# Optimization experiments

Measured on AMD Instinct MI355X. Metric: run time of the kernel, lower is better.

## Reference

```python
import math
import jax, jax.numpy as jnp
import numpy as np

B, S, D, H = 4, 1024, 512, 8
DK = D // H


def lin(x, W, b):
    # torch nn.Linear: y = x @ W.T + b, W: [out, in]
    return jnp.einsum('...i,oi->...o', x, W) + b


def layer_norm(x, scale, bias, eps=1e-5):
    m = jnp.mean(x, axis=-1, keepdims=True)
    v = jnp.var(x, axis=-1, keepdims=True)
    return (x - m) / jnp.sqrt(v + eps) * scale + bias


def mha(q_in, k_in, v_in, Wq, bq, Wk, bk, Wv, bv, Wo, bo, gammas, mask, zero_pad):
    b, s, _ = q_in.shape
    q = lin(q_in, Wq, bq).reshape(b, s, H, DK).transpose(0, 2, 1, 3)  # bhsd
    k = lin(k_in, Wk, bk).reshape(b, s, H, DK).transpose(0, 2, 1, 3)
    v = lin(v_in, Wv, bv).reshape(b, s, H, DK).transpose(0, 2, 1, 3)
    scores = jnp.einsum('bhid,bhjd->bhij', q, k) / math.sqrt(DK)
    # no-grad distance-decay branch
    s_ = jnp.where(mask, scores, jnp.float32(-1e32))
    s_ = jax.nn.softmax(s_, axis=-1) * mask
    distcum = jnp.cumsum(s_, axis=-1)
    disttotal = jnp.sum(s_, axis=-1, keepdims=True)
    idx = jnp.arange(s)
    pos = jnp.abs(idx[None, :] - idx[:, None]).astype(jnp.float32)[None, None]  # |i-j|
    dist = jax.lax.stop_gradient(jnp.sqrt(jnp.clip((disttotal - distcum) * pos, 0.0, None)))
    gamma = -jax.nn.softplus(gammas)[None]  # [1,h,1,1]
    total_effect = jnp.clip(jnp.exp(dist * gamma), 1e-5, 1e5)
    scores = scores * total_effect
    # NOTE: original code calls scores.masked_fill(...) without assignment (no-op);
    # faithfully NOT re-masking before this softmax.
    att = jax.nn.softmax(scores, axis=-1)
    if zero_pad:
        att = att.at[:, :, 0, :].set(0.0)
    out = jnp.einsum('bhij,bhjd->bhid', att, v).transpose(0, 2, 1, 3).reshape(b, s, D)
    return lin(out, Wo, bo)


def setup_inputs() -> dict:
    key = jax.random.key(0)
    ks = jax.random.split(key, 32)
    ki = iter(range(32))

    def w(shape, scale=0.02):
        return jax.random.normal(ks[next(ki)], shape, jnp.float32) * scale

    inp = {
        'q_emb': jax.random.normal(ks[next(ki)], (B, S, D), jnp.float32),
        'qa_emb': jax.random.normal(ks[next(ki)], (B, S, D), jnp.float32),
    }
    for blk in (1, 2, 3):
        inp[f'Wq{blk}'] = w((D, D)); inp[f'bq{blk}'] = jnp.zeros((D,), jnp.float32)
        if blk == 3:
            inp['Wk3'] = w((D, D)); inp['bk3'] = jnp.zeros((D,), jnp.float32)
        inp[f'Wv{blk}'] = w((D, D)); inp[f'bv{blk}'] = jnp.zeros((D,), jnp.float32)
        inp[f'Wo{blk}'] = w((D, D)); inp[f'bo{blk}'] = jnp.zeros((D,), jnp.float32)
        inp[f'g{blk}'] = w((H, 1, 1), 0.5)
        inp[f'ls{blk}'] = jnp.ones((D,), jnp.float32)
        inp[f'lb{blk}'] = jnp.zeros((D,), jnp.float32)
    inp['know'] = jax.random.uniform(ks[next(ki)], (1, 1, D), jnp.float32, -1.0, 1.0)
    inp['Wlk'] = w((D, DK)); inp['b_lk'] = jnp.zeros((D,), jnp.float32)
    inp['Wlv'] = w((D, DK)); inp['b_lv'] = jnp.zeros((D,), jnp.float32)
    return inp


def reference(q_emb, qa_emb,
              Wq1, bq1, Wv1, bv1, Wo1, bo1, g1, ls1, lb1,
              Wq2, bq2, Wv2, bv2, Wo2, bo2, g2, ls2, lb2,
              Wq3, bq3, Wk3, bk3, Wv3, bv3, Wo3, bo3, g3, ls3, lb3,
              know, Wlk, b_lk, Wlv, b_lv):
    b, s, d = q_emb.shape
    ones = jnp.ones((s, s), dtype=bool)
    mask_peek = jnp.tril(ones, k=0)[None, None]   # peek_cur=True
    mask_nopeek = jnp.tril(ones, k=-1)[None, None]  # peek_cur=False

    # block1 / block2 share k and q projections (kq_same=True)
    hq = layer_norm(q_emb + mha(q_emb, q_emb, q_emb, Wq1, bq1, Wq1, bq1,
                                Wv1, bv1, Wo1, bo1, g1, mask_peek, False), ls1, lb1)
    ha = layer_norm(qa_emb + mha(qa_emb, qa_emb, qa_emb, Wq2, bq2, Wq2, bq2,
                                 Wv2, bv2, Wo2, bo2, g2, mask_peek, False), ls2, lb2)
    query = jnp.broadcast_to(know, (b, s, d))
    h = layer_norm(query + mha(query, hq, ha, Wq3, bq3, Wk3, bk3,
                               Wv3, bv3, Wo3, bo3, g3, mask_nopeek, True), ls3, lb3)

    # small multi-head combine
    key_t = jax.nn.sigmoid(lin(query.reshape(b, s, H, DK), Wlk, b_lk))  # [b,s,h,d]
    val_t = jax.nn.sigmoid(lin(h.reshape(b, s, H, DK), Wlv, b_lv))     # [b,s,h,d]
    beta = jnp.einsum('bshd,bsd->bsh', key_t, q_emb)
    alpha = jax.nn.softmax(beta, axis=-1)
    out = jnp.einsum('bsh,bshd->bsd', alpha, val_t)
    return out
```

## Files before the change

### kernel.cpp

```cpp
#include <hip/hip_runtime.h>
#include <math.h>

#define BB 4
#define S 1024
#define D 512
#define H 8
#define DKH 64

#define ATT_LD 1032
#define LOG2E 1.4426950408889634f

typedef __attribute__((ext_vector_type(8))) short bf16x8;
typedef __attribute__((ext_vector_type(4))) float f32x4;

__device__ __forceinline__ unsigned short f2bf(float f){
  unsigned int u = __float_as_uint(f);
  u += 0x7FFFu + ((u >> 16) & 1u);
  return (unsigned short)(u >> 16);
}
__device__ __forceinline__ float bf2f(unsigned int v){
  return __uint_as_float(v << 16);
}
__device__ __forceinline__ f32x4 MFMA(bf16x8 a, bf16x8 b, f32x4 c){
  return __builtin_amdgcn_mfma_f32_16x16x32_bf16(a, b, c, 0, 0, 0);
}
__device__ __forceinline__ void gl_lds16(const void* g, void* l){
  __builtin_amdgcn_global_load_lds(
      (const __attribute__((address_space(1))) void*)g,
      (__attribute__((address_space(3))) void*)l, 16, 0, 0);
}

__device__ __forceinline__ float blk_sum(float* r, int t, float v){
  r[t] = v; __syncthreads();
  for (int s = 128; s > 0; s >>= 1){
    if (t < s) r[t] += r[t + s];
    __syncthreads();
  }
  float res = r[0]; __syncthreads();
  return res;
}

struct GemmJobs {
  const unsigned short* A[4];
  const unsigned short* W[4];
  const float* bias[4];
  void* C[4];
};
template<int OUTBF>
__global__ __launch_bounds__(256) void mfma_gemm_b(GemmJobs jb)
{
  __shared__ __align__(16) short As[128][32];
  __shared__ __align__(16) short Ws[128][32];
  const int t = threadIdx.x;
  const int z = blockIdx.z;
  const int n0 = blockIdx.x * 128, m0 = blockIdx.y * 128;
  const unsigned short* A = jb.A[z];
  const unsigned short* W = jb.W[z];
  const float* bias = jb.bias[z];
  const int w = t >> 6, lane = t & 63;
  const int wm = (w >> 1) << 6, wn = (w & 1) << 6;
  const int lm = lane & 15, q = lane >> 4;
  const int r = t >> 2, cc = (t & 3) << 3;
  char* ldsA = ((char*)&As[0][0]) + w * 1024;
  char* ldsW = ((char*)&Ws[0][0]) + w * 1024;
  f32x4 acc[4][4];
  #pragma unroll
  for (int a_ = 0; a_ < 4; a_++)
    #pragma unroll
    for (int b_ = 0; b_ < 4; b_++)
      acc[a_][b_] = (f32x4){0.f, 0.f, 0.f, 0.f};
  for (int k0 = 0; k0 < D; k0 += 32){
    gl_lds16(&A[(size_t)(m0 + r)      * D + k0 + cc], ldsA);
    gl_lds16(&A[(size_t)(m0 + r + 64) * D + k0 + cc], ldsA + 4096);
    gl_lds16(&W[(size_t)(n0 + r)      * D + k0 + cc], ldsW);
    gl_lds16(&W[(size_t)(n0 + r + 64) * D + k0 + cc], ldsW + 4096);
    __syncthreads();
    bf16x8 af[4], bf[4];
    #pragma unroll
    for (int mt = 0; mt < 4; mt++) af[mt] = *(const bf16x8*)&As[wm + mt*16 + lm][q*8];
    #pragma unroll
    for (int nt = 0; nt < 4; nt++) bf[nt] = *(const bf16x8*)&Ws[wn + nt*16 + lm][q*8];
    #pragma unroll
    for (int mt = 0; mt < 4; mt++)
      #pragma unroll
      for (int nt = 0; nt < 4; nt++)
        acc[mt][nt] = MFMA(af[mt], bf[nt], acc[mt][nt]);
    __syncthreads();
  }
  #pragma unroll
  for (int nt = 0; nt < 4; nt++){
    const int n = n0 + wn + nt*16 + lm;
    const float bs = bias[n];
    #pragma unroll
    for (int mt = 0; mt < 4; mt++){
      const int mb = m0 + wm + mt*16 + (q << 2);
      f32x4 c = acc[mt][nt];
      #pragma unroll
      for (int rr = 0; rr < 4; rr++){
        float vv = c[rr] + bs;
        if (OUTBF)
          ((unsigned short*)jb.C[z])[(size_t)(mb + rr) * D + n] = f2bf(vv);
        else
          ((float*)jb.C[z])[(size_t)(mb + rr) * D + n] = vv;
      }
    }
  }
}

#define KS_LD 66
struct VTArgs { const unsigned short* v[2]; unsigned short* vt[2]; };
__global__ __launch_bounds__(256) void vt_kernel(VTArgs a)
{
  __shared__ unsigned short tile[64 * KS_LD];
  const int z = blockIdx.z, bh = blockIdx.y, b = bh >> 3, h = bh & 7;
  const int j0 = blockIdx.x * 64;
  const int t = threadIdx.x;
  const unsigned short* vp = a.v[z];
  unsigned short* vtp = a.vt[z] + (size_t)bh * 64 * S;
  #pragma unroll
  for (int p = 0; p < 2; p++){
    int lin = t + p * 256, row = lin >> 3, c8 = (lin & 7) << 3;
    *(uint4*)&tile[row * KS_LD + c8] =
      *(const uint4*)&vp[((size_t)b * S + j0 + row) * D + h * DKH + c8];
  }
  __syncthreads();
  #pragma unroll
  for (int p = 0; p < 2; p++){
    int lin = t + p * 256, d = lin >> 3, c8 = (lin & 7) << 3;
    unsigned short tmp[8];
    #pragma unroll
    for (int jx = 0; jx < 8; jx++) tmp[jx] = tile[(c8 + jx) * KS_LD + d];
    *(uint4*)&vtp[(size_t)d * S + j0 + c8] = *(const uint4*)tmp;
  }
}

struct FAArgs {
  const unsigned short* qk[2];
  const unsigned short* vt[2];
  unsigned short* ctx[2];
  const float* g[2];
  const float* c3;
  int diag, zero_pad;
};
template<int C3>
__global__ __launch_bounds__(256) void fused_attn(FAArgs a)
{
  __shared__ __align__(16) unsigned short att[16 * ATT_LD];
  const int t = threadIdx.x;
  const int z = blockIdx.z;
  const int bh = blockIdx.y, b = bh >> 3, h = bh & 7;
  const int i0 = blockIdx.x * 16;
  const int w = t >> 6, lane = t & 63, lm = lane & 15, q = lane >> 4;
  const unsigned short* qkp = a.qk[z];
  const unsigned short* vtp = a.vt[z] + (size_t)bh * 64 * S;
  unsigned short* ctxp = a.ctx[z];
  float gm2;
  { float gv = a.g[z][h];
    gm2 = -((gv > 20.f) ? gv : log1pf(expf(gv))) * LOG2E; }

  if (!C3){
    bf16x8 af0 = *(const bf16x8*)&qkp[((size_t)b * S + i0 + lm) * D + h * DKH + q*8];
    bf16x8 af1 = *(const bf16x8*)&qkp[((size_t)b * S + i0 + lm) * D + h * DKH + 32 + q*8];
    for (int jc = 0; jc < S; jc += 64){
      const int jrow = jc + w*16 + lm;
      const size_t kb = ((size_t)b * S + jrow) * D + h * DKH;
      bf16x8 bv0 = *(const bf16x8*)&qkp[kb + q*8];
      bf16x8 bv1 = *(const bf16x8*)&qkp[kb + 32 + q*8];
      f32x4 acc = (f32x4){0.f, 0.f, 0.f, 0.f};
      acc = MFMA(af0, bv0, acc);
      acc = MFMA(af1, bv1, acc);
      #pragma unroll
      for (int rr = 0; rr < 4; rr++)
        att[(q*4 + rr) * ATT_LD + jc + w*16 + lm] = f2bf(acc[rr] * 0.125f);
    }
  }
  __syncthreads();

  const int jA0 = lane * 8, jB0 = 512 + lane * 8;
  for (int rloc = 0; rloc < 4; rloc++){
    const int i = i0 + w*4 + rloc;
    unsigned short* rowp = &att[(w*4 + rloc) * ATT_LD];
    if (C3 && a.zero_pad && i == 0){
      uint4 zz = make_uint4(0u,0u,0u,0u);
      *(uint4*)&rowp[jA0] = zz;
      *(uint4*)&rowp[jB0] = zz;
      continue;
    }
    float c[16];
    if (C3){
      const float* c3p = a.c3 + ((size_t)b * H + h) * S;
      #pragma unroll
      for (int sg = 0; sg < 2; sg++)
        #pragma unroll
        for (int p4 = 0; p4 < 2; p4++){
          float4 x = *(const float4*)&c3p[sg*512 + lane*8 + p4*4];
          c[sg*8+p4*4+0] = x.x * LOG2E; c[sg*8+p4*4+1] = x.y * LOG2E;
          c[sg*8+p4*4+2] = x.z * LOG2E; c[sg*8+p4*4+3] = x.w * LOG2E;
        }
    } else {
      #pragma unroll
      for (int sg = 0; sg < 2; sg++){
        uint4 u = *(const uint4*)&rowp[sg*512 + lane*8];
        unsigned int uu[4] = {u.x, u.y, u.z, u.w};
        #pragma unroll
        for (int mel = 0; mel < 4; mel++){
          c[sg*8 + mel*2]     = bf2f(uu[mel] & 0xffffu) * LOG2E;
          c[sg*8 + mel*2 + 1] = bf2f(uu[mel] >> 16) * LOG2E;
        }
      }
    }
    const int jmax = i + a.diag;
    float pl[16];
    float runA = 0.f, runB = 0.f;
    #pragma unroll
    for (int k = 0; k < 8; k++){
      float e = (jA0 + k <= jmax) ? exp2f(c[k]) : 0.f;
      runA += e; pl[k] = runA;
    }
    #pragma unroll
    for (int k = 0; k < 8; k++){
      float e = (jB0 + k <= jmax) ? exp2f(c[8+k]) : 0.f;
      runB += e; pl[8+k] = runB;
    }
    float sA = runA, sB = runB;
    #pragma unroll
    for (int off = 1; off < 64; off <<= 1){
      float uA = __shfl_up(sA, off, 64);
      float uB = __shfl_up(sB, off, 64);
      if (lane >= off){ sA += uA; sB += uB; }
    }
    const float TA = __shfl(sA, 63, 64);
    const float T  = TA + __shfl(sB, 63, 64);
    const float inv1 = 1.f / T;
    const float cbaseA = (T - (sA - runA)) * inv1;
    const float cbaseB = (T - (TA + sB - runB)) * inv1;
    const float fiA = (float)(i - jA0);
    const float fiB = (float)(i - jB0);
    float ls2 = 0.f;
    #pragma unroll
    for (int k = 0; k < 8; k++){
      float remn = fmaf(-pl[k], inv1, cbaseA);
      float pos  = fabsf(fiA - (float)k);
      float dist = sqrtf(fmaxf(remn * pos, 0.f));
      float eff  = fmaxf(exp2f(gm2 * dist), 1e-5f);
      float pp   = exp2f(c[k] * eff);
      ls2 += pp; pl[k] = pp;
    }
    #pragma unroll
    for (int k = 0; k < 8; k++){
      float remn = fmaf(-pl[8+k], inv1, cbaseB);
      float pos  = fabsf(fiB - (float)k);
      float dist = sqrtf(fmaxf(remn * pos, 0.f));
      float eff  = fmaxf(exp2f(gm2 * dist), 1e-5f);
      float pp   = exp2f(c[8+k] * eff);
      ls2 += pp; pl[8+k] = pp;
    }
    #pragma unroll
    for (int off = 1; off < 64; off <<= 1) ls2 += __shfl_xor(ls2, off, 64);
    const float inv2 = 1.f / ls2;
    #pragma unroll
    for (int sg = 0; sg < 2; sg++){
      unsigned int ou[4];
      #pragma unroll
      for (int mel = 0; mel < 4; mel++){
        unsigned int lo = f2bf(pl[sg*8 + 2*mel]     * inv2);
        unsigned int hi = f2bf(pl[sg*8 + 2*mel + 1] * inv2);
        ou[mel] = lo | (hi << 16);
      }
      *(uint4*)&rowp[sg*512 + lane*8] = make_uint4(ou[0], ou[1], ou[2], ou[3]);
    }
  }
  __syncthreads();

  f32x4 acc = (f32x4){0.f,0.f,0.f,0.f};
  for (int kc = 0; kc < S; kc += 64){
    #pragma unroll
    for (int kft = 0; kft < 2; kft++){
      bf16x8 afv = *(const bf16x8*)&att[lm * ATT_LD + kc + kft*32 + q*8];
      bf16x8 bv  = *(const bf16x8*)&vtp[(size_t)(w*16 + lm) * S + kc + kft*32 + q*8];
      acc = MFMA(afv, bv, acc);
    }
  }
  #pragma unroll
  for (int rr = 0; rr < 4; rr++){
    const int row = i0 + q*4 + rr;
    ctxp[((size_t)b * S + row) * D + h * DKH + w*16 + lm] = f2bf(acc[rr]);
  }
}

__global__ __launch_bounds__(256) void ln_residual(
    const float* __restrict__ resid, const float* __restrict__ y,
    const float* __restrict__ ls, const float* __restrict__ lb,
    unsigned short* __restrict__ out, int bcast)
{
  const int r = blockIdx.x, t = threadIdx.x;
  __shared__ float red[256];
  const size_t base = (size_t)r * D;
  float r0 = bcast ? resid[t]       : resid[base + t];
  float r1 = bcast ? resid[t + 256] : resid[base + t + 256];
  float x0 = r0 + y[base + t];
  float x1 = r1 + y[base + t + 256];
  float mean = blk_sum(red, t, x0 + x1) * (1.0f / 512.0f);
  float d0 = x0 - mean, d1 = x1 - mean;
  float var = blk_sum(red, t, d0*d0 + d1*d1) * (1.0f / 512.0f);
  float inv = rsqrtf(var + 1e-5f);
  out[base + t]       = f2bf(d0 * inv * ls[t]       + lb[t]);
  out[base + t + 256] = f2bf(d1 * inv * ls[t + 256] + lb[t + 256]);
}

struct CvtJobs {
  const float* s[12];
  unsigned short* d[12];
  int n[12];
};
__global__ __launch_bounds__(256) void cvt_all(CvtJobs jb){
  const int z = blockIdx.y;
  const int n = jb.n[z];
  const float* s = jb.s[z];
  unsigned short* d = jb.d[z];
  for (int idx = blockIdx.x * 256 + threadIdx.x; idx < n; idx += gridDim.x * 256)
    d[idx] = f2bf(s[idx]);
}

__global__ __launch_bounds__(256) void qvec3_kernel(
    const float* __restrict__ know, const float* __restrict__ Wq3,
    const float* __restrict__ bq3, float* __restrict__ q3)
{
  const int wv = (blockIdx.x * 256 + threadIdx.x) >> 6;
  const int lane = threadIdx.x & 63;
  const float* wr = Wq3 + (size_t)wv * 512 + lane * 8;
  const float* kr = know + lane * 8;
  float4 w0 = *(const float4*)&wr[0], w1 = *(const float4*)&wr[4];
  float4 k0 = *(const float4*)&kr[0], k1 = *(const float4*)&kr[4];
  float p = w0.x*k0.x + w0.y*k0.y + w0.z*k0.z + w0.w*k0.w
          + w1.x*k1.x + w1.y*k1.y + w1.z*k1.z + w1.w*k1.w;
  #pragma unroll
  for (int off = 1; off < 64; off <<= 1) p += __shfl_xor(p, off, 64);
  if (lane == 0) q3[wv] = p + bq3[wv];
}

__global__ __launch_bounds__(256) void keyt_kernel(
    const float* __restrict__ know, const float* __restrict__ Wlk,
    const float* __restrict__ blk_, float* __restrict__ keyt)
{
  int idx = blockIdx.x * 256 + threadIdx.x;
  int h = idx >> 9, n = idx & 511;
  float acc = 0.f;
  for (int i = 0; i < 64; i++) acc += know[h * 64 + i] * Wlk[(size_t)n * 64 + i];
  keyt[idx] = 1.f / (1.f + __expf(-(acc + blk_[n])));
}

__global__ __launch_bounds__(256) void scores3_kernel(
    const float* __restrict__ q3, const unsigned short* __restrict__ k3,
    float* __restrict__ c3)
{
  int idx = blockIdx.x * 256 + threadIdx.x;
  int j  = idx & (S - 1);
  int bh = idx >> 10;
  int h  = bh & 7, b = bh >> 3;
  const unsigned short* kp = k3 + ((size_t)b * S + j) * D + h * DKH;
  const float* qp = q3 + h * DKH;
  float acc = 0.f;
  #pragma unroll
  for (int d8 = 0; d8 < 64; d8 += 8){
    uint4 u = *(const uint4*)&kp[d8];
    unsigned int uu[4] = {u.x, u.y, u.z, u.w};
    #pragma unroll
    for (int mel = 0; mel < 4; mel++){
      acc += qp[d8 + 2*mel]     * bf2f(uu[mel] & 0xffffu);
      acc += qp[d8 + 2*mel + 1] * bf2f(uu[mel] >> 16);
    }
  }
  c3[idx] = acc * 0.125f;
}

__global__ __launch_bounds__(256) void alphas_kernel(
    const float* __restrict__ keyt, const float* __restrict__ q_emb,
    float* __restrict__ alpha)
{
  const int row = blockIdx.x * 4 + (threadIdx.x >> 6);
  const int l = threadIdx.x & 63;
  const int h = l >> 3, sub = l & 7;
  const float* qr = q_emb + (size_t)row * D;
  const float* kt = keyt + h * D;
  float p = 0.f;
  for (int d = sub; d < D; d += 8) p += kt[d] * qr[d];
  p += __shfl_xor(p, 1, 64);
  p += __shfl_xor(p, 2, 64);
  p += __shfl_xor(p, 4, 64);
  float m = p;
  m = fmaxf(m, __shfl_xor(m, 8, 64));
  m = fmaxf(m, __shfl_xor(m, 16, 64));
  m = fmaxf(m, __shfl_xor(m, 32, 64));
  float e = __expf(p - m);
  float ssum = e;
  ssum += __shfl_xor(ssum, 8, 64);
  ssum += __shfl_xor(ssum, 16, 64);
  ssum += __shfl_xor(ssum, 32, 64);
  if (sub == 0) alpha[(size_t)row * H + h] = e / ssum;
}

__global__ __launch_bounds__(256) void val_fused(
    const unsigned short* __restrict__ Ah,
    const unsigned short* __restrict__ Wv,
    const float* __restrict__ blv,
    const float* __restrict__ alpha,
    float* __restrict__ out)
{
  __shared__ __align__(16) short As[128][32];
  __shared__ __align__(16) short Ws[128][32];
  __shared__ float als[128];
  const int t = threadIdx.x;
  const int n0 = blockIdx.x * 128, m0 = blockIdx.y * 128;
  if (t < 128) als[t] = alpha[m0 + t];
  const int w = t >> 6, lane = t & 63;
  const int wm = (w >> 1) << 6, wn = (w & 1) << 6;
  const int lm = lane & 15, q = lane >> 4;
  const int r = t >> 2, cc = (t & 3) << 3;
  f32x4 acc[4][4];
  #pragma unroll
  for (int a_ = 0; a_ < 4; a_++)
    #pragma unroll
    for (int b_ = 0; b_ < 4; b_++)
      acc[a_][b_] = (f32x4){0.f, 0.f, 0.f, 0.f};
  for (int k0 = 0; k0 < 64; k0 += 32){
    *(uint4*)&As[r][cc]      = *(const uint4*)&Ah[(size_t)(m0 + r) * 64 + k0 + cc];
    *(uint4*)&As[r + 64][cc] = *(const uint4*)&Ah[(size_t)(m0 + r + 64) * 64 + k0 + cc];
    *(uint4*)&Ws[r][cc]      = *(const uint4*)&Wv[(size_t)(n0 + r) * 64 + k0 + cc];
    *(uint4*)&Ws[r + 64][cc] = *(const uint4*)&Wv[(size_t)(n0 + r + 64) * 64 + k0 + cc];
    __syncthreads();
    bf16x8 af[4], bf[4];
    #pragma unroll
    for (int mt = 0; mt < 4; mt++) af[mt] = *(const bf16x8*)&As[wm + mt*16 + lm][q*8];
    #pragma unroll
    for (int nt = 0; nt < 4; nt++) bf[nt] = *(const bf16x8*)&Ws[wn + nt*16 + lm][q*8];
    #pragma unroll
    for (int mt = 0; mt < 4; mt++)
      #pragma unroll
      for (int nt = 0; nt < 4; nt++)
        acc[mt][nt] = MFMA(af[mt], bf[nt], acc[mt][nt]);
    __syncthreads();
  }
  #pragma unroll
  for (int nt = 0; nt < 4; nt++){
    const int n = n0 + wn + nt*16 + lm;
    const float bs = blv[n];
    #pragma unroll
    for (int mt = 0; mt < 4; mt++){
      const int mb = m0 + wm + mt*16;
      f32x4 c = acc[mt][nt];
      float part = 0.f;
      #pragma unroll
      for (int rr = 0; rr < 4; rr++){
        const int ml = (mb - m0) + (q << 2) + rr;
        float sg = 1.f / (1.f + __expf(-(c[rr] + bs)));
        part += als[ml] * sg;
      }
      part += __shfl_xor(part, 16, 64);
      if ((q & 1) == 0){
        const int srow = (mb >> 3) + (q >> 1);
        out[(size_t)srow * D + n] = part;
      }
    }
  }
}

extern "C" void kernel_launch(void* const* d_in, const int* in_sizes, int n_in,
                              void* d_out, int out_size, void* d_ws, size_t ws_size,
                              hipStream_t stream) {
  const float* q_emb  = (const float*)d_in[0];
  const float* qa_emb = (const float*)d_in[1];
  const float* Wq1 = (const float*)d_in[2],  *bq1 = (const float*)d_in[3];
  const float* Wv1 = (const float*)d_in[4],  *bv1 = (const float*)d_in[5];
  const float* Wo1 = (const float*)d_in[6],  *bo1 = (const float*)d_in[7];
  const float* g1  = (const float*)d_in[8],  *ls1 = (const float*)d_in[9],  *lb1 = (const float*)d_in[10];
  const float* Wq2 = (const float*)d_in[11], *bq2 = (const float*)d_in[12];
  const float* Wv2 = (const float*)d_in[13], *bv2 = (const float*)d_in[14];
  const float* Wo2 = (const float*)d_in[15], *bo2 = (const float*)d_in[16];
  const float* g2  = (const float*)d_in[17], *ls2 = (const float*)d_in[18], *lb2 = (const float*)d_in[19];
  const float* Wq3 = (const float*)d_in[20], *bq3 = (const float*)d_in[21];
  const float* Wk3 = (const float*)d_in[22], *bk3 = (const float*)d_in[23];
  const float* Wv3 = (const float*)d_in[24], *bv3 = (const float*)d_in[25];
  const float* Wo3 = (const float*)d_in[26], *bo3 = (const float*)d_in[27];
  const float* g3  = (const float*)d_in[28], *ls3 = (const float*)d_in[29], *lb3 = (const float*)d_in[30];
  const float* know = (const float*)d_in[31];
  const float* Wlk  = (const float*)d_in[32], *b_lk = (const float*)d_in[33];
  const float* Wlv  = (const float*)d_in[34], *b_lv = (const float*)d_in[35];
  float* outp = (float*)d_out;

  const size_t NSD = (size_t)BB * S * D;
  unsigned short* p = (unsigned short*)d_ws;
  unsigned short* qk1b = p; p += NSD;
  unsigned short* v1b  = p; p += NSD;
  unsigned short* qk2b = p; p += NSD;
  unsigned short* v2b  = p; p += NSD;
  unsigned short* k3b  = p; p += NSD;
  unsigned short* v3b  = p; p += NSD;
  unsigned short* ctx1b= p; p += NSD;
  unsigned short* ctx2b= p; p += NSD;
  unsigned short* ctx3b= p; p += NSD;
  unsigned short* xqb  = p; p += NSD;
  unsigned short* xab  = p; p += NSD;
  unsigned short* hqb  = p; p += NSD;
  unsigned short* hab  = p; p += NSD;
  unsigned short* hfb  = p; p += NSD;
  unsigned short* vt1  = p; p += NSD;
  unsigned short* vt2  = p; p += NSD;
  unsigned short* vt3  = p; p += NSD;
  unsigned short* wb   = p; p += (size_t)9 * D * D;
  unsigned short* wlvb = p; p += (size_t)D * DKH;
  float* yv0   = (float*)p;
  float* yv1   = yv0 + NSD;
  float* q3    = yv1 + NSD;
  float* keyt  = q3 + 512;
  float* c3    = keyt + 4096;
  float* alpha = c3 + (size_t)BB * H * S;

  unsigned short* Wq1b = wb + 0*(size_t)D*D;
  unsigned short* Wv1b = wb + 1*(size_t)D*D;
  unsigned short* Wo1b = wb + 2*(size_t)D*D;
  unsigned short* Wq2b = wb + 3*(size_t)D*D;
  unsigned short* Wv2b = wb + 4*(size_t)D*D;
  unsigned short* Wo2b = wb + 5*(size_t)D*D;
  unsigned short* Wk3b = wb + 6*(size_t)D*D;
  unsigned short* Wv3b = wb + 7*(size_t)D*D;
  unsigned short* Wo3b = wb + 8*(size_t)D*D;

  CvtJobs jb;
  jb.s[0] = q_emb;  jb.d[0] = xqb;  jb.n[0] = (int)NSD;
  jb.s[1] = qa_emb; jb.d[1] = xab;  jb.n[1] = (int)NSD;
  jb.s[2] = Wq1; jb.d[2] = Wq1b; jb.n[2] = D*D;
  jb.s[3] = Wv1; jb.d[3] = Wv1b; jb.n[3] = D*D;
  jb.s[4] = Wo1; jb.d[4] = Wo1b; jb.n[4] = D*D;
  jb.s[5] = Wq2; jb.d[5] = Wq2b; jb.n[5] = D*D;
  jb.s[6] = Wv2; jb.d[6] = Wv2b; jb.n[6] = D*D;
  jb.s[7] = Wo2; jb.d[7] = Wo2b; jb.n[7] = D*D;
  jb.s[8] = Wk3; jb.d[8] = Wk3b; jb.n[8] = D*D;
  jb.s[9] = Wv3; jb.d[9] = Wv3b; jb.n[9] = D*D;
  jb.s[10] = Wo3; jb.d[10] = Wo3b; jb.n[10] = D*D;
  jb.s[11] = Wlv; jb.d[11] = wlvb; jb.n[11] = D*DKH;
  cvt_all<<<dim3(256, 12), 256, 0, stream>>>(jb);

  {
    GemmJobs g;
    g.A[0]=xqb; g.W[0]=Wq1b; g.bias[0]=bq1; g.C[0]=qk1b;
    g.A[1]=xqb; g.W[1]=Wv1b; g.bias[1]=bv1; g.C[1]=v1b;
    g.A[2]=xab; g.W[2]=Wq2b; g.bias[2]=bq2; g.C[2]=qk2b;
    g.A[3]=xab; g.W[3]=Wv2b; g.bias[3]=bv2; g.C[3]=v2b;
    mfma_gemm_b<1><<<dim3(4, 32, 4), 256, 0, stream>>>(g);
  }
  { VTArgs a; a.v[0]=v1b; a.v[1]=v2b; a.vt[0]=vt1; a.vt[1]=vt2;
    vt_kernel<<<dim3(16, 32, 2), 256, 0, stream>>>(a); }
  { FAArgs a;
    a.qk[0]=qk1b; a.qk[1]=qk2b; a.vt[0]=vt1; a.vt[1]=vt2;
    a.ctx[0]=ctx1b; a.ctx[1]=ctx2b; a.g[0]=g1; a.g[1]=g2;
    a.c3=nullptr; a.diag=0; a.zero_pad=0;
    fused_attn<0><<<dim3(64, 32, 2), 256, 0, stream>>>(a); }
  {
    GemmJobs g;
    g.A[0]=ctx1b; g.W[0]=Wo1b; g.bias[0]=bo1; g.C[0]=yv0;
    g.A[1]=ctx2b; g.W[1]=Wo2b; g.bias[1]=bo2; g.C[1]=yv1;
    g.A[2]=ctx1b; g.W[2]=Wo1b; g.bias[2]=bo1; g.C[2]=yv0;
    g.A[3]=ctx1b; g.W[3]=Wo1b; g.bias[3]=bo1; g.C[3]=yv0;
    mfma_gemm_b<0><<<dim3(4, 32, 2), 256, 0, stream>>>(g);
  }
  ln_residual<<<BB*S, 256, 0, stream>>>(q_emb,  yv0, ls1, lb1, hqb, 0);
  ln_residual<<<BB*S, 256, 0, stream>>>(qa_emb, yv1, ls2, lb2, hab, 0);

  qvec3_kernel<<<128, 256, 0, stream>>>(know, Wq3, bq3, q3);
  {
    GemmJobs g;
    g.A[0]=hqb; g.W[0]=Wk3b; g.bias[0]=bk3; g.C[0]=k3b;
    g.A[1]=hab; g.W[1]=Wv3b; g.bias[1]=bv3; g.C[1]=v3b;
    g.A[2]=hqb; g.W[2]=Wk3b; g.bias[2]=bk3; g.C[2]=k3b;
    g.A[3]=hqb; g.W[3]=Wk3b; g.bias[3]=bk3; g.C[3]=k3b;
    mfma_gemm_b<1><<<dim3(4, 32, 2), 256, 0, stream>>>(g);
  }
  { VTArgs a; a.v[0]=v3b; a.v[1]=v3b; a.vt[0]=vt3; a.vt[1]=vt3;
    vt_kernel<<<dim3(16, 32, 1), 256, 0, stream>>>(a); }
  scores3_kernel<<<128, 256, 0, stream>>>(q3, k3b, c3);
  { FAArgs a;
    a.qk[0]=k3b; a.qk[1]=k3b; a.vt[0]=vt3; a.vt[1]=vt3;
    a.ctx[0]=ctx3b; a.ctx[1]=ctx3b; a.g[0]=g3; a.g[1]=g3;
    a.c3=c3; a.diag=-1; a.zero_pad=1;
    fused_attn<1><<<dim3(64, 32, 1), 256, 0, stream>>>(a); }
  {
    GemmJobs g;
    g.A[0]=ctx3b; g.W[0]=Wo3b; g.bias[0]=bo3; g.C[0]=yv0;
    g.A[1]=ctx3b; g.W[1]=Wo3b; g.bias[1]=bo3; g.C[1]=yv0;
    g.A[2]=ctx3b; g.W[2]=Wo3b; g.bias[2]=bo3; g.C[2]=yv0;
    g.A[3]=ctx3b; g.W[3]=Wo3b; g.bias[3]=bo3; g.C[3]=yv0;
    mfma_gemm_b<0><<<dim3(4, 32, 1), 256, 0, stream>>>(g);
  }
  ln_residual<<<BB*S, 256, 0, stream>>>(know, yv0, ls3, lb3, hfb, 1);

  keyt_kernel<<<16, 256, 0, stream>>>(know, Wlk, b_lk, keyt);
  alphas_kernel<<<1024, 256, 0, stream>>>(keyt, q_emb, alpha);
  val_fused<<<dim3(4, 256), 256, 0, stream>>>(hfb, wlvb, b_lv, alpha, outp);
}
```

Measured before the change: 478.8 us.

## Streamline decay softmax: skip masked half, defer normalization, batch small kernels

Inside fused attention, the upper-half scan and decay evaluation are skipped when the causal row limit lies below column 512. The row normalization is deferred to the attention-times-V epilogue through a shared per-row reciprocal, and faster bf16 rounding, hardware exp2/sqrt/rcp intrinsics and hoisted C3 exponentials are used. Separately, the two layer-norm launches are batched into one grid and the q3/keyt kernels are merged into a single launch to cut launch overhead. The skipped half writes unnormalized exp values instead of decayed ones, which could alter results, and the approximate intrinsics and round-half-up conversion change numerics slightly.

```diff
diff --git a/kernel.cpp b/kernel.cpp
--- a/kernel.cpp
+++ b/kernel.cpp
@@ -13,10 +13,38 @@
 typedef __attribute__((ext_vector_type(8))) short bf16x8;
 typedef __attribute__((ext_vector_type(4))) float f32x4;
 
+#if __has_builtin(__builtin_amdgcn_exp2f)
+#define EXP2(x) __builtin_amdgcn_exp2f(x)
+#else
+#define EXP2(x) exp2f(x)
+#endif
+#if __has_builtin(__builtin_amdgcn_sqrtf)
+#define SQRTF(x) __builtin_amdgcn_sqrtf(x)
+#else
+#define SQRTF(x) sqrtf(x)
+#endif
+#if __has_builtin(__builtin_amdgcn_rcpf)
+#define RCPF(x) __builtin_amdgcn_rcpf(x)
+#else
+#define RCPF(x) (1.0f / (x))
+#endif
+
 __device__ __forceinline__ unsigned short f2bf(float f){
   unsigned int u = __float_as_uint(f);
   u += 0x7FFFu + ((u >> 16) & 1u);
   return (unsigned short)(u >> 16);
+}
+__device__ __forceinline__ unsigned short f2bf_rhu(float f){
+  return (unsigned short)((__float_as_uint(f) + 0x8000u) >> 16);
+}
+__device__ __forceinline__ unsigned int pk_rhu(float lo, float hi){
+  unsigned int a = __float_as_uint(lo) + 0x8000u;
+  unsigned int b = __float_as_uint(hi) + 0x8000u;
+#if __has_builtin(__builtin_amdgcn_perm)
+  return __builtin_amdgcn_perm(b, a, 0x07060302u);
+#else
+  return (a >> 16) | (b & 0xffff0000u);
+#endif
 }
 __device__ __forceinline__ float bf2f(unsigned int v){
   return __uint_as_float(v << 16);
@@ -146,6 +174,7 @@
 __global__ __launch_bounds__(256) void fused_attn(FAArgs a)
 {
   __shared__ __align__(16) unsigned short att[16 * ATT_LD];
+  __shared__ float ls2s[16];
   const int t = threadIdx.x;
   const int z = blockIdx.z;
   const int bh = blockIdx.y, b = bh >> 3, h = bh & 7;
@@ -171,33 +200,119 @@
       acc = MFMA(af1, bv1, acc);
       #pragma unroll
       for (int rr = 0; rr < 4; rr++)
-        att[(q*4 + rr) * ATT_LD + jc + w*16 + lm] = f2bf(acc[rr] * 0.125f);
+        att[(q*4 + rr) * ATT_LD + jc + w*16 + lm] = f2bf_rhu(acc[rr] * 0.125f);
     }
   }
   __syncthreads();
 
   const int jA0 = lane * 8, jB0 = 512 + lane * 8;
+
+  float cH[16], erH[16];
+  if (C3){
+    const float* c3p = a.c3 + ((size_t)b * H + h) * S;
+    #pragma unroll
+    for (int sg = 0; sg < 2; sg++)
+      #pragma unroll
+      for (int p4 = 0; p4 < 2; p4++){
+        float4 x = *(const float4*)&c3p[sg*512 + lane*8 + p4*4];
+        cH[sg*8+p4*4+0] = x.x * LOG2E; cH[sg*8+p4*4+1] = x.y * LOG2E;
+        cH[sg*8+p4*4+2] = x.z * LOG2E; cH[sg*8+p4*4+3] = x.w * LOG2E;
+      }
+    #pragma unroll
+    for (int k = 0; k < 16; k++) erH[k] = EXP2(cH[k]);
+  }
+
+  auto decay_row = [&](const float (&c)[16], const float (&er)[16],
+                       const int i, unsigned short* rowp, const int rl){
+    const int jmax = i + a.diag;
+    const bool skipB = (jmax < 512);
+    float pl[16];
+    float runA = 0.f;
+    #pragma unroll
+    for (int k = 0; k < 8; k++){
+      float e = (jA0 + k <= jmax) ? er[k] : 0.f;
+      runA += e; pl[k] = runA;
+    }
+    float sA = runA;
+    #pragma unroll
+    for (int off = 1; off < 64; off <<= 1){
+      float u = __shfl_up(sA, off, 64);
+      if (lane >= off) sA += u;
+    }
+    const float TA = __shfl(sA, 63, 64);
+    float T = TA, sB = 0.f, runB = 0.f;
+    if (!skipB){
+      #pragma unroll
+      for (int k = 0; k < 8; k++){
+        float e = (jB0 + k <= jmax) ? er[8+k] : 0.f;
+        runB += e; pl[8+k] = runB;
+      }
+      sB = runB;
+      #pragma unroll
+      for (int off = 1; off < 64; off <<= 1){
+        float u = __shfl_up(sB, off, 64);
+        if (lane >= off) sB += u;
+      }
+      T = TA + __shfl(sB, 63, 64);
+    }
+    const float inv1 = RCPF(T);
+    const float cbaseA = (T - (sA - runA)) * inv1;
+    const float fiA = (float)(i - jA0);
+    float ls2 = 0.f;
+    #pragma unroll
+    for (int k = 0; k < 8; k++){
+      float remn = fmaf(-pl[k], inv1, cbaseA);
+      float pos  = fabsf(fiA - (float)k);
+      float dist = SQRTF(fmaxf(remn * pos, 0.f));
+      float eff  = fmaxf(EXP2(gm2 * dist), 1e-5f);
+      float pp   = EXP2(c[k] * eff);
+      ls2 += pp; pl[k] = pp;
+    }
+    if (!skipB){
+      const float cbaseB = (T - (TA + sB - runB)) * inv1;
+      const float fiB = (float)(i - jB0);
+      #pragma unroll
+      for (int k = 0; k < 8; k++){
+        float remn = fmaf(-pl[8+k], inv1, cbaseB);
+        float pos  = fabsf(fiB - (float)k);
+        float dist = SQRTF(fmaxf(remn * pos, 0.f));
+        float eff  = fmaxf(EXP2(gm2 * dist), 1e-5f);
+        float pp   = EXP2(c[8+k] * eff);
+        ls2 += pp; pl[8+k] = pp;
+      }
+    } else {
+      #pragma unroll
+      for (int k = 0; k < 8; k++){ pl[8+k] = er[8+k]; ls2 += er[8+k]; }
+    }
+    #pragma unroll
+    for (int off = 1; off < 64; off <<= 1) ls2 += __shfl_xor(ls2, off, 64);
+    if (lane == 0) ls2s[rl] = RCPF(ls2);
+    #pragma unroll
+    for (int sg = 0; sg < 2; sg++){
+      uint4 o;
+      o.x = pk_rhu(pl[sg*8+0], pl[sg*8+1]);
+      o.y = pk_rhu(pl[sg*8+2], pl[sg*8+3]);
+      o.z = pk_rhu(pl[sg*8+4], pl[sg*8+5]);
+      o.w = pk_rhu(pl[sg*8+6], pl[sg*8+7]);
+      *(uint4*)&rowp[sg*512 + lane*8] = o;
+    }
+  };
+
   for (int rloc = 0; rloc < 4; rloc++){
-    const int i = i0 + w*4 + rloc;
-    unsigned short* rowp = &att[(w*4 + rloc) * ATT_LD];
+    const int rl = w*4 + rloc;
+    const int i = i0 + rl;
+    unsigned short* rowp = &att[rl * ATT_LD];
     if (C3 && a.zero_pad && i == 0){
       uint4 zz = make_uint4(0u,0u,0u,0u);
       *(uint4*)&rowp[jA0] = zz;
       *(uint4*)&rowp[jB0] = zz;
+      if (lane == 0) ls2s[0] = 1.f;
       continue;
     }
-    float c[16];
     if (C3){
-      const float* c3p = a.c3 + ((size_t)b * H + h) * S;
-      #pragma unroll
-      for (int sg = 0; sg < 2; sg++)
-        #pragma unroll
-        for (int p4 = 0; p4 < 2; p4++){
-          float4 x = *(const float4*)&c3p[sg*512 + lane*8 + p4*4];
-          c[sg*8+p4*4+0] = x.x * LOG2E; c[sg*8+p4*4+1] = x.y * LOG2E;
-          c[sg*8+p4*4+2] = x.z * LOG2E; c[sg*8+p4*4+3] = x.w * LOG2E;
-        }
+      decay_row(cH, erH, i, rowp, rl);
     } else {
+      float c[16], er[16];
       #pragma unroll
       for (int sg = 0; sg < 2; sg++){
         uint4 u = *(const uint4*)&rowp[sg*512 + lane*8];
@@ -208,66 +323,9 @@
           c[sg*8 + mel*2 + 1] = bf2f(uu[mel] >> 16) * LOG2E;
         }
       }
-    }
-    const int jmax = i + a.diag;
-    float pl[16];
-    float runA = 0.f, runB = 0.f;
-    #pragma unroll
-    for (int k = 0; k < 8; k++){
-      float e = (jA0 + k <= jmax) ? exp2f(c[k]) : 0.f;
-      runA += e; pl[k] = runA;
-    }
-    #pragma unroll
-    for (int k = 0; k < 8; k++){
-      float e = (jB0 + k <= jmax) ? exp2f(c[8+k]) : 0.f;
-      runB += e; pl[8+k] = runB;
-    }
-    float sA = runA, sB = runB;
-    #pragma unroll
-    for (int off = 1; off < 64; off <<= 1){
-      float uA = __shfl_up(sA, off, 64);
-      float uB = __shfl_up(sB, off, 64);
-      if (lane >= off){ sA += uA; sB += uB; }
-    }
-    const float TA = __shfl(sA, 63, 64);
-    const float T  = TA + __shfl(sB, 63, 64);
-    const float inv1 = 1.f / T;
-    const float cbaseA = (T - (sA - runA)) * inv1;
-    const float cbaseB = (T - (TA + sB - runB)) * inv1;
-    const float fiA = (float)(i - jA0);
-    const float fiB = (float)(i - jB0);
-    float ls2 = 0.f;
-    #pragma unroll
-    for (int k = 0; k < 8; k++){
-      float remn = fmaf(-pl[k], inv1, cbaseA);
-      float pos  = fabsf(fiA - (float)k);
-      float dist = sqrtf(fmaxf(remn * pos, 0.f));
-      float eff  = fmaxf(exp2f(gm2 * dist), 1e-5f);
-      float pp   = exp2f(c[k] * eff);
-      ls2 += pp; pl[k] = pp;
-    }
-    #pragma unroll
-    for (int k = 0; k < 8; k++){
-      float remn = fmaf(-pl[8+k], inv1, cbaseB);
-      float pos  = fabsf(fiB - (float)k);
-      float dist = sqrtf(fmaxf(remn * pos, 0.f));
-      float eff  = fmaxf(exp2f(gm2 * dist), 1e-5f);
-      float pp   = exp2f(c[8+k] * eff);
-      ls2 += pp; pl[8+k] = pp;
-    }
-    #pragma unroll
-    for (int off = 1; off < 64; off <<= 1) ls2 += __shfl_xor(ls2, off, 64);
-    const float inv2 = 1.f / ls2;
-    #pragma unroll
-    for (int sg = 0; sg < 2; sg++){
-      unsigned int ou[4];
-      #pragma unroll
-      for (int mel = 0; mel < 4; mel++){
-        unsigned int lo = f2bf(pl[sg*8 + 2*mel]     * inv2);
-        unsigned int hi = f2bf(pl[sg*8 + 2*mel + 1] * inv2);
-        ou[mel] = lo | (hi << 16);
-      }
-      *(uint4*)&rowp[sg*512 + lane*8] = make_uint4(ou[0], ou[1], ou[2], ou[3]);
+      #pragma unroll
+      for (int k = 0; k < 16; k++) er[k] = EXP2(c[k]);
+      decay_row(c, er, i, rowp, rl);
     }
   }
   __syncthreads();
@@ -283,19 +341,30 @@
   }
   #pragma unroll
   for (int rr = 0; rr < 4; rr++){
-    const int row = i0 + q*4 + rr;
-    ctxp[((size_t)b * S + row) * D + h * DKH + w*16 + lm] = f2bf(acc[rr]);
-  }
-}
-
-__global__ __launch_bounds__(256) void ln_residual(
-    const float* __restrict__ resid, const float* __restrict__ y,
-    const float* __restrict__ ls, const float* __restrict__ lb,
-    unsigned short* __restrict__ out, int bcast)
-{
+    const int rl = q*4 + rr;
+    const float sc = ls2s[rl];
+    const int row = i0 + rl;
+    ctxp[((size_t)b * S + row) * D + h * DKH + w*16 + lm] = f2bf(acc[rr] * sc);
+  }
+}
+
+struct LNJobs {
+  const float* resid[2];
+  const float* y[2];
+  const float* ls[2];
+  const float* lb[2];
+  unsigned short* out[2];
+  int bcast[2];
+};
+__global__ __launch_bounds__(256) void ln_residual_b(LNJobs j)
+{
+  const int z = blockIdx.y;
   const int r = blockIdx.x, t = threadIdx.x;
   __shared__ float red[256];
   const size_t base = (size_t)r * D;
+  const float* resid = j.resid[z];
+  const float* y = j.y[z];
+  const int bcast = j.bcast[z];
   float r0 = bcast ? resid[t]       : resid[base + t];
   float r1 = bcast ? resid[t + 256] : resid[base + t + 256];
   float x0 = r0 + y[base + t];
@@ -304,8 +373,8 @@
   float d0 = x0 - mean, d1 = x1 - mean;
   float var = blk_sum(red, t, d0*d0 + d1*d1) * (1.0f / 512.0f);
   float inv = rsqrtf(var + 1e-5f);
-  out[base + t]       = f2bf(d0 * inv * ls[t]       + lb[t]);
-  out[base + t + 256] = f2bf(d1 * inv * ls[t + 256] + lb[t + 256]);
+  j.out[z][base + t]       = f2bf(d0 * inv * j.ls[z][t]       + j.lb[z][t]);
+  j.out[z][base + t + 256] = f2bf(d1 * inv * j.ls[z][t + 256] + j.lb[z][t + 256]);
 }
 
 struct CvtJobs {
@@ -322,32 +391,31 @@
     d[idx] = f2bf(s[idx]);
 }
 
-__global__ __launch_bounds__(256) void qvec3_kernel(
+__global__ __launch_bounds__(256) void know_kernel(
     const float* __restrict__ know, const float* __restrict__ Wq3,
-    const float* __restrict__ bq3, float* __restrict__ q3)
-{
-  const int wv = (blockIdx.x * 256 + threadIdx.x) >> 6;
-  const int lane = threadIdx.x & 63;
-  const float* wr = Wq3 + (size_t)wv * 512 + lane * 8;
-  const float* kr = know + lane * 8;
-  float4 w0 = *(const float4*)&wr[0], w1 = *(const float4*)&wr[4];
-  float4 k0 = *(const float4*)&kr[0], k1 = *(const float4*)&kr[4];
-  float p = w0.x*k0.x + w0.y*k0.y + w0.z*k0.z + w0.w*k0.w
-          + w1.x*k1.x + w1.y*k1.y + w1.z*k1.z + w1.w*k1.w;
-  #pragma unroll
-  for (int off = 1; off < 64; off <<= 1) p += __shfl_xor(p, off, 64);
-  if (lane == 0) q3[wv] = p + bq3[wv];
-}
-
-__global__ __launch_bounds__(256) void keyt_kernel(
-    const float* __restrict__ know, const float* __restrict__ Wlk,
-    const float* __restrict__ blk_, float* __restrict__ keyt)
-{
-  int idx = blockIdx.x * 256 + threadIdx.x;
-  int h = idx >> 9, n = idx & 511;
-  float acc = 0.f;
-  for (int i = 0; i < 64; i++) acc += know[h * 64 + i] * Wlk[(size_t)n * 64 + i];
-  keyt[idx] = 1.f / (1.f + __expf(-(acc + blk_[n])));
+    const float* __restrict__ bq3, float* __restrict__ q3,
+    const float* __restrict__ Wlk, const float* __restrict__ blk_,
+    float* __restrict__ keyt)
+{
+  if (blockIdx.x < 128){
+    const int wv = (blockIdx.x * 256 + threadIdx.x) >> 6;
+    const int lane = threadIdx.x & 63;
+    const float* wr = Wq3 + (size_t)wv * 512 + lane * 8;
+    const float* kr = know + lane * 8;
+    float4 w0 = *(const float4*)&wr[0], w1 = *(const float4*)&wr[4];
+    float4 k0 = *(const float4*)&kr[0], k1 = *(const float4*)&kr[4];
+    float p = w0.x*k0.x + w0.y*k0.y + w0.z*k0.z + w0.w*k0.w
+            + w1.x*k1.x + w1.y*k1.y + w1.z*k1.z + w1.w*k1.w;
+    #pragma unroll
+    for (int off = 1; off < 64; off <<= 1) p += __shfl_xor(p, off, 64);
+    if (lane == 0) q3[wv] = p + bq3[wv];
+  } else {
+    int idx = (blockIdx.x - 128) * 256 + threadIdx.x;
+    int h = idx >> 9, n = idx & 511;
+    float acc = 0.f;
+    for (int i = 0; i < 64; i++) acc += know[h * 64 + i] * Wlk[(size_t)n * 64 + i];
+    keyt[idx] = 1.f / (1.f + __expf(-(acc + blk_[n])));
+  }
 }
 
 __global__ __launch_bounds__(256) void scores3_kernel(
@@ -564,10 +632,14 @@
     g.A[3]=ctx1b; g.W[3]=Wo1b; g.bias[3]=bo1; g.C[3]=yv0;
     mfma_gemm_b<0><<<dim3(4, 32, 2), 256, 0, stream>>>(g);
   }
-  ln_residual<<<BB*S, 256, 0, stream>>>(q_emb,  yv0, ls1, lb1, hqb, 0);
-  ln_residual<<<BB*S, 256, 0, stream>>>(qa_emb, yv1, ls2, lb2, hab, 0);
-
-  qvec3_kernel<<<128, 256, 0, stream>>>(know, Wq3, bq3, q3);
+  {
+    LNJobs lj;
+    lj.resid[0]=q_emb;  lj.y[0]=yv0; lj.ls[0]=ls1; lj.lb[0]=lb1; lj.out[0]=hqb; lj.bcast[0]=0;
+    lj.resid[1]=qa_emb; lj.y[1]=yv1; lj.ls[1]=ls2; lj.lb[1]=lb2; lj.out[1]=hab; lj.bcast[1]=0;
+    ln_residual_b<<<dim3(BB*S, 2), 256, 0, stream>>>(lj);
+  }
+
+  know_kernel<<<144, 256, 0, stream>>>(know, Wq3, bq3, q3, Wlk, b_lk, keyt);
   {
     GemmJobs g;
     g.A[0]=hqb; g.W[0]=Wk3b; g.bias[0]=bk3; g.C[0]=k3b;
@@ -592,9 +664,13 @@
     g.A[3]=ctx3b; g.W[3]=Wo3b; g.bias[3]=bo3; g.C[3]=yv0;
     mfma_gemm_b<0><<<dim3(4, 32, 1), 256, 0, stream>>>(g);
   }
-  ln_residual<<<BB*S, 256, 0, stream>>>(know, yv0, ls3, lb3, hfb, 1);
-
-  keyt_kernel<<<16, 256, 0, stream>>>(know, Wlk, b_lk, keyt);
+  {
+    LNJobs lj;
+    lj.resid[0]=know; lj.y[0]=yv0; lj.ls[0]=ls3; lj.lb[0]=lb3; lj.out[0]=hfb; lj.bcast[0]=1;
+    lj.resid[1]=know; lj.y[1]=yv0; lj.ls[1]=ls3; lj.lb[1]=lb3; lj.out[1]=hfb; lj.bcast[1]=1;
+    ln_residual_b<<<dim3(BB*S, 1), 256, 0, stream>>>(lj);
+  }
+
   alphas_kernel<<<1024, 256, 0, stream>>>(keyt, q_emb, alpha);
   val_fused<<<dim3(4, 256), 256, 0, stream>>>(hfb, wlvb, b_lv, alpha, outp);
 }
```

Measured after the change: 438.9 us. -8.3%, faster.
